# Optimization experiments

Measured on AMD Instinct MI355X. Metric: run time of the kernel, lower is better.

The kernel has to match this reference:

```python
import jax, jax.numpy as jnp
import numpy as np

B, T, C, H, W = 8, 8, 32, 16, 28
NH, DK = 4, 8                 # n_head, d_k == d_v
RADIUS = [3, 3, 3, 3]
DILATION = [1, 3, 5, 7]
LN_EPS = 1e-5


def setup_inputs() -> dict:
    key = jax.random.key(0)
    ks = jax.random.split(key, 8)
    s = 1.0 / np.sqrt(C).astype(np.float32)
    return {
        "first": jax.random.normal(ks[0], (B, T, C, H, W), jnp.float32),
        "x": jax.random.normal(ks[1], (B, T, C, H, W), jnp.float32),
        "Wq": jax.random.normal(ks[2], (NH * DK, C), jnp.float32) * s,
        "Wk": jax.random.normal(ks[3], (NH * DK, C), jnp.float32) * s,
        "Wv": jax.random.normal(ks[4], (NH * DK, C), jnp.float32) * s,
        "Wo": jax.random.normal(ks[5], (C, NH * DK), jnp.float32) * s,
        "ln_gamma": 1.0 + 0.1 * jax.random.normal(ks[6], (DK, H, W), jnp.float32),
        "ln_beta": 0.1 * jax.random.normal(ks[7], (DK, H, W), jnp.float32),
    }


def _shift(x, dy, dx):
    # out[..., i, j] = x[..., i+dy, j+dx]; zero out-of-bounds. mask: (H, W) valid.
    h, w = x.shape[-2:]
    xs = jnp.roll(x, (-dy, -dx), axis=(-2, -1))
    mh = (jnp.arange(h) + dy >= 0) & (jnp.arange(h) + dy < h)
    mw = (jnp.arange(w) + dx >= 0) & (jnp.arange(w) + dx < w)
    m = mh[:, None] & mw[None, :]
    return jnp.where(m, xs, 0.0), m


def _head_attn(q, k, v, radius, dilation, scale):
    # q,k,v: (b,t,c,h,w). Returns softmaxed scores P (b,t,O*t,h,w) and
    # aggregation T (b,t,c,h,w). Aggregation uses RAW scaled scores (as the repo
    # does: spatial_temporal_aggregation receives M_A_i, not its softmax).
    b, t, c, h, w = q.shape
    scores, vals, masks = [], [], []
    for dy in range(-radius, radius + 1):
        for dx in range(-radius, radius + 1):
            ks, m = _shift(k, dy * dilation, dx * dilation)
            vs, _ = _shift(v, dy * dilation, dx * dilation)
            # score against all source frames s at the shifted spatial location
            scores.append(jnp.einsum('btchw,bschw->btshw', q, ks))
            vals.append(vs)
            masks.append(m)
    A = jnp.stack(scores, axis=2)                      # (b,t,O,s,h,w), O=(2r+1)^2
    M = jnp.stack(masks, axis=0)                       # (O,h,w)
    A = jnp.where(M[None, None, :, None], A / scale, -jnp.inf)
    O = A.shape[2]
    P = jax.nn.softmax(A.reshape(b, t, O * t, h, w), axis=2)
    Wm = jnp.where(M[None, None, :, None], A, 0.0)     # skip invalid (-inf) slots
    V = jnp.stack(vals, axis=0)                        # (O,b,s,c,h,w)
    Tout = jnp.einsum('btoshw,obschw->btchw', Wm, V)
    return P, Tout


def reference(first, x, Wq, Wk, Wv, Wo, ln_gamma, ln_beta):
    b, t, c, h, w = x.shape
    q = jnp.einsum('btchw,oc->btohw', first, Wq).reshape(b, t, NH, DK, h, w)
    k = jnp.einsum('btchw,oc->btohw', x, Wk).reshape(b, t, NH, DK, h, w)
    v = jnp.einsum('btchw,oc->btohw', x, Wv).reshape(b, t, NH, DK, h, w)
    scale = float(np.sqrt(C / NH))
    Ps, Ts = [], []
    for i in range(NH):
        qi = q[:, :, i]
        mu = jnp.mean(qi, axis=(2, 3, 4), keepdims=True)
        var = jnp.var(qi, axis=(2, 3, 4), keepdims=True)
        qi = (qi - mu) / jnp.sqrt(var + LN_EPS) * ln_gamma + ln_beta
        P, Ti = _head_attn(qi, k[:, :, i], v[:, :, i], RADIUS[i], DILATION[i], scale)
        Ps.append(P)
        Ts.append(Ti)
    M_S = jnp.max(jnp.concatenate(Ps, axis=2), axis=2)   # (b,t,h,w)
    M_T = jnp.concatenate(Ts, axis=2)                    # (b,t,NH*DK,h,w)
    out = jnp.einsum('btchw,oc->btohw', M_T, Wo) * M_S[:, :, None]
    return out
```

## Files before the change

kernel.cpp:

```cpp
#include <hip/hip_runtime.h>

#define Bc 8
#define Tc 8
#define Cc 32
#define Hc 16
#define Wc 28
#define NHc 4
#define DKc 8
#define HWc (Hc*Wc)
#define INV_SCALE 0.35355339059327373f
#define LN_EPSc 1e-5f

typedef _Float16 half8  __attribute__((ext_vector_type(8)));
typedef _Float16 half2v __attribute__((ext_vector_type(2)));

union H8 { half8 v; half2v h2[4]; };


__global__ __launch_bounds__(448) void qkv_ln_kernel(
    const float* __restrict__ first, const float* __restrict__ x,
    const float* __restrict__ Wq, const float* __restrict__ Wk,
    const float* __restrict__ Wv,
    const float* __restrict__ gamma, const float* __restrict__ beta,
    half8* __restrict__ Qh, half8* __restrict__ Kh, float* __restrict__ V)
{
    int blk  = blockIdx.x;
    int head = blk >> 6;
    int bt   = blk & 63;
    int t    = bt % Tc;
    int b    = bt / Tc;
    int tid  = threadIdx.x;

    const float* fp = first + (size_t)bt * Cc * HWc + tid;
    const float* xp = x     + (size_t)bt * Cc * HWc + tid;
    float fv[Cc], xv[Cc];
#pragma unroll
    for (int c = 0; c < Cc; ++c) { fv[c] = fp[c*HWc]; xv[c] = xp[c*HWc]; }

    float qv[DKc], kv[DKc], vv[DKc];
#pragma unroll
    for (int dk = 0; dk < DKc; ++dk) {
        int o = head*DKc + dk;
        float aq = 0.f, ak = 0.f, av = 0.f;
#pragma unroll
        for (int c = 0; c < Cc; ++c) {
            aq = fmaf(Wq[o*Cc+c], fv[c], aq);
            ak = fmaf(Wk[o*Cc+c], xv[c], ak);
            av = fmaf(Wv[o*Cc+c], xv[c], av);
        }
        qv[dk] = aq; kv[dk] = ak; vv[dk] = av;
    }

    int bh = b*NHc + head;
    half8 kh;
#pragma unroll
    for (int dk = 0; dk < DKc; ++dk) kh[dk] = (_Float16)kv[dk];
    Kh[((size_t)bh*Tc + t)*HWc + tid] = kh;

    float* vp = V + (((size_t)bh*Tc + t)*HWc + tid)*DKc;
    *(float4*)(vp)   = make_float4(vv[0],vv[1],vv[2],vv[3]);
    *(float4*)(vp+4) = make_float4(vv[4],vv[5],vv[6],vv[7]);

    float s1 = 0.f, s2 = 0.f;
#pragma unroll
    for (int dk = 0; dk < DKc; ++dk) { s1 += qv[dk]; s2 += qv[dk]*qv[dk]; }
#pragma unroll
    for (int off = 32; off >= 1; off >>= 1) {
        s1 += __shfl_down(s1, off, 64);
        s2 += __shfl_down(s2, off, 64);
    }
    __shared__ float r1[8], r2[8];
    int wid = tid >> 6, lane = tid & 63;
    if (lane == 0) { r1[wid] = s1; r2[wid] = s2; }
    __syncthreads();
    float S1 = 0.f, S2 = 0.f;
#pragma unroll
    for (int wv2 = 0; wv2 < 7; ++wv2) { S1 += r1[wv2]; S2 += r2[wv2]; }
    const float invN = 1.f / (float)(DKc * HWc);
    float mu   = S1 * invN;
    float var  = S2 * invN - mu*mu;
    float rstd = rsqrtf(var + LN_EPSc);

    half8 qh;
#pragma unroll
    for (int dk = 0; dk < DKc; ++dk) {
        float gg = gamma[dk*HWc + tid];
        float bb = beta [dk*HWc + tid];
        qh[dk] = (_Float16)(((qv[dk] - mu) * rstd * gg + bb) * INV_SCALE);
    }
    Qh[((size_t)bh*Tc + t)*HWc + tid] = qh;
}

__global__ __launch_bounds__(448, 4) void attn_kernel(
    const half8* __restrict__ Qh, const half8* __restrict__ Kh,
    const float* __restrict__ V,
    half8* __restrict__ Tpart, float2* __restrict__ LMpart)
{
    int blk = blockIdx.x;
    int p   = blk >> 8;
    int i   = blk & 255;
    int b   = i >> 5;
    int ha  = (i >> 4) & 1;
    int s   = (i >> 1) & 7;
    int th  = i & 1;

    int head = p ? (3 - ha) : ha;
    int dil  = 2*head + 1;
    int bh   = b*NHc + head;
    int t0   = th*4;

    int tid = threadIdx.x;
    int w = tid % Wc;
    int h = tid / Wc;

    __shared__ half8  sK [HWc+1];
    __shared__ float4 sV0[HWc+1], sV1[HWc+1];

    sK[tid] = Kh[((size_t)bh*Tc + s)*HWc + tid];
    const float* vp = V + ((size_t)bh*Tc + s)*HWc*DKc;
    sV0[tid] = *(const float4*)(vp + tid*DKc);
    sV1[tid] = *(const float4*)(vp + tid*DKc + 4);
    if (tid == 0) {
        half8 z = {};
        sK[HWc]  = z;
        sV0[HWc] = make_float4(0.f,0.f,0.f,0.f);
        sV1[HWc] = make_float4(0.f,0.f,0.f,0.f);
    }

    H8 q[4];
#pragma unroll
    for (int j = 0; j < 4; ++j)
        q[j].v = Qh[((size_t)bh*Tc + (t0+j))*HWc + tid];

    float4 a0[4], a1[4];
    float l[4], m[4];
#pragma unroll
    for (int j = 0; j < 4; ++j) {
        a0[j] = make_float4(0.f,0.f,0.f,0.f);
        a1[j] = make_float4(0.f,0.f,0.f,0.f);
        l[j] = 0.f; m[j] = -1e30f;
    }

    __syncthreads();

    for (int dy = -3; dy <= 3; ++dy) {
        int hy = h + dy*dil;
        if ((unsigned)hy >= (unsigned)Hc) continue;
        int rowbase = hy*Wc;
#pragma unroll
        for (int dx = -3; dx <= 3; ++dx) {
            int wx = w + dx*dil;
            bool cv = (unsigned)wx < (unsigned)Wc;
            int idx = cv ? (rowbase + wx) : HWc;
            float bias = cv ? 0.f : -1e30f;
            H8 k; k.v = sK[idx];
            float4 v0 = sV0[idx], v1 = sV1[idx];
#pragma unroll
            for (int j = 0; j < 4; ++j) {
                float sc = __builtin_amdgcn_fdot2(q[j].h2[0], k.h2[0],
                           __builtin_amdgcn_fdot2(q[j].h2[1], k.h2[1],
                           __builtin_amdgcn_fdot2(q[j].h2[2], k.h2[2],
                           __builtin_amdgcn_fdot2(q[j].h2[3], k.h2[3],
                                                  0.f, false), false), false), false);
                float msc = sc + bias;
                m[j] = fmaxf(m[j], msc);
                l[j] += __expf(msc);
                a0[j].x = fmaf(sc, v0.x, a0[j].x);
                a0[j].y = fmaf(sc, v0.y, a0[j].y);
                a0[j].z = fmaf(sc, v0.z, a0[j].z);
                a0[j].w = fmaf(sc, v0.w, a0[j].w);
                a1[j].x = fmaf(sc, v1.x, a1[j].x);
                a1[j].y = fmaf(sc, v1.y, a1[j].y);
                a1[j].z = fmaf(sc, v1.z, a1[j].z);
                a1[j].w = fmaf(sc, v1.w, a1[j].w);
            }
        }
    }

    half8*  tp  = Tpart  + (size_t)(bh*Tc + s)*Tc*HWc + tid;
    float2* lmp = LMpart + (size_t)(bh*Tc + s)*Tc*HWc + tid;
#pragma unroll
    for (int j = 0; j < 4; ++j) {
        half8 hv;
        hv[0] = (_Float16)a0[j].x; hv[1] = (_Float16)a0[j].y;
        hv[2] = (_Float16)a0[j].z; hv[3] = (_Float16)a0[j].w;
        hv[4] = (_Float16)a1[j].x; hv[5] = (_Float16)a1[j].y;
        hv[6] = (_Float16)a1[j].z; hv[7] = (_Float16)a1[j].w;
        tp [(t0+j)*HWc] = hv;
        lmp[(t0+j)*HWc] = make_float2(l[j], m[j]);
    }
}

__global__ __launch_bounds__(448) void outproj_kernel(
    const half8* __restrict__ Tpart, const float2* __restrict__ LMpart,
    const float* __restrict__ Wo, float* __restrict__ out)
{
    int blk = blockIdx.x;
    int og  = blk >> 6;
    int bt  = blk & 63;
    int b   = bt >> 3, t = bt & 7;
    int tid = threadIdx.x;

    float mv[Cc];
    float MS = 0.f;
#pragma unroll
    for (int head = 0; head < NHc; ++head) {
        int bh = b*NHc + head;
        float acc[DKc];
#pragma unroll
        for (int j = 0; j < DKc; ++j) acc[j] = 0.f;
        float lsum = 0.f, mmax = -1e30f;
#pragma unroll
        for (int s = 0; s < Tc; ++s) {
            half8 u = Tpart[(size_t)((bh*Tc + s)*Tc + t)*HWc + tid];
#pragma unroll
            for (int j = 0; j < DKc; ++j) acc[j] += (float)u[j];
            float2 lm = LMpart[(size_t)((bh*Tc + s)*Tc + t)*HWc + tid];
            lsum += lm.x; mmax = fmaxf(mmax, lm.y);
        }
#pragma unroll
        for (int j = 0; j < DKc; ++j) mv[head*DKc + j] = acc[j];
        MS = fmaxf(MS, __expf(mmax) / lsum);
    }
#pragma unroll
    for (int i = 0; i < 8; ++i) {
        int o = og*8 + i;
        float a = 0.f;
#pragma unroll
        for (int c = 0; c < Cc; ++c) a = fmaf(Wo[o*Cc+c], mv[c], a);
        out[((size_t)bt*Cc + o)*HWc + tid] = a * MS;
    }
}

extern "C" void kernel_launch(void* const* d_in, const int* in_sizes, int n_in,
                              void* d_out, int out_size, void* d_ws, size_t ws_size,
                              hipStream_t stream) {
    const float* first = (const float*)d_in[0];
    const float* x     = (const float*)d_in[1];
    const float* Wq    = (const float*)d_in[2];
    const float* Wk    = (const float*)d_in[3];
    const float* Wv    = (const float*)d_in[4];
    const float* Wo    = (const float*)d_in[5];
    const float* g     = (const float*)d_in[6];
    const float* bta   = (const float*)d_in[7];
    float* out = (float*)d_out;

    float* ws = (float*)d_ws;
    const size_t N5 = (size_t)Bc*NHc*Tc*HWc*DKc;
    half8*  Qh  = (half8*)ws;
    half8*  Kh  = (half8*)(ws + N5/2);
    float*  V   = ws + N5;
    half8*  Tp  = (half8*)(ws + 2*N5);
    float2* LMp = (float2*)(ws + 6*N5);

    qkv_ln_kernel <<<Bc*Tc*NHc, 448, 0, stream>>>(first, x, Wq, Wk, Wv, g, bta, Qh, Kh, V);
    attn_kernel   <<<512,       448, 0, stream>>>(Qh, Kh, V, Tp, LMp);
    outproj_kernel<<<256,       448, 0, stream>>>(Tp, LMp, Wo, out);
}
```

Baseline: 116.0 us.

## Pad shared K/V with zero halo, template dilation, use exp2 and fp16 V

Stores K/V in a zero-padded shared-memory grid so out-of-range horizontal neighbours read zeros, which removes the per-tap bounds check and the -inf bias. The extra exp2(0)=1 terms this adds to the softmax denominator are subtracted analytically using a per-pixel count of invalid taps. The dilation becomes a template parameter so offsets are compile-time constants and the dy loop is fully unrolled. Q is prescaled by log2e so exp2 can be used, with a ln2 factor applied back on the aggregated output, and V is written in fp16 to halve its traffic. The risks are reduced V precision, a larger padded shared-memory footprint that may lower occupancy, and a larger code size from four template instantiations.

```diff
diff --git a/kernel.cpp b/kernel.cpp
--- a/kernel.cpp
+++ b/kernel.cpp
@@ -9,7 +9,18 @@
 #define DKc 8
 #define HWc (Hc*Wc)
 #define INV_SCALE 0.35355339059327373f
+#define LOG2E 1.4426950408889634f
+#define LN2f 0.6931471805599453f
 #define LN_EPSc 1e-5f
+
+#define WPAD 70
+#define NSLOT (Hc*WPAD)
+
+#if __has_builtin(__builtin_amdgcn_exp2f)
+#define EXP2f(x) __builtin_amdgcn_exp2f(x)
+#else
+#define EXP2f(x) exp2f(x)
+#endif
 
 typedef _Float16 half8  __attribute__((ext_vector_type(8)));
 typedef _Float16 half2v __attribute__((ext_vector_type(2)));
@@ -22,7 +33,7 @@
     const float* __restrict__ Wq, const float* __restrict__ Wk,
     const float* __restrict__ Wv,
     const float* __restrict__ gamma, const float* __restrict__ beta,
-    half8* __restrict__ Qh, half8* __restrict__ Kh, float* __restrict__ V)
+    half8* __restrict__ Qh, half8* __restrict__ Kh, half8* __restrict__ Vh)
 {
     int blk  = blockIdx.x;
     int head = blk >> 6;
@@ -52,14 +63,14 @@
     }
 
     int bh = b*NHc + head;
-    half8 kh;
-#pragma unroll
-    for (int dk = 0; dk < DKc; ++dk) kh[dk] = (_Float16)kv[dk];
+    half8 kh, vh;
+#pragma unroll
+    for (int dk = 0; dk < DKc; ++dk) {
+        kh[dk] = (_Float16)kv[dk];
+        vh[dk] = (_Float16)vv[dk];
+    }
     Kh[((size_t)bh*Tc + t)*HWc + tid] = kh;
-
-    float* vp = V + (((size_t)bh*Tc + t)*HWc + tid)*DKc;
-    *(float4*)(vp)   = make_float4(vv[0],vv[1],vv[2],vv[3]);
-    *(float4*)(vp+4) = make_float4(vv[4],vv[5],vv[6],vv[7]);
+    Vh[((size_t)bh*Tc + t)*HWc + tid] = vh;
 
     float s1 = 0.f, s2 = 0.f;
 #pragma unroll
@@ -81,80 +92,76 @@
     float var  = S2 * invN - mu*mu;
     float rstd = rsqrtf(var + LN_EPSc);
 
+    const float QSCALE = INV_SCALE * LOG2E;
     half8 qh;
 #pragma unroll
     for (int dk = 0; dk < DKc; ++dk) {
         float gg = gamma[dk*HWc + tid];
         float bb = beta [dk*HWc + tid];
-        qh[dk] = (_Float16)(((qv[dk] - mu) * rstd * gg + bb) * INV_SCALE);
+        qh[dk] = (_Float16)(((qv[dk] - mu) * rstd * gg + bb) * QSCALE);
     }
     Qh[((size_t)bh*Tc + t)*HWc + tid] = qh;
 }
 
-__global__ __launch_bounds__(448, 4) void attn_kernel(
+template<int DIL>
+__device__ __forceinline__ void attn_body(
+    int bh, int s, int t0, int tid,
     const half8* __restrict__ Qh, const half8* __restrict__ Kh,
-    const float* __restrict__ V,
-    half8* __restrict__ Tpart, float2* __restrict__ LMpart)
-{
-    int blk = blockIdx.x;
-    int p   = blk >> 8;
-    int i   = blk & 255;
-    int b   = i >> 5;
-    int ha  = (i >> 4) & 1;
-    int s   = (i >> 1) & 7;
-    int th  = i & 1;
-
-    int head = p ? (3 - ha) : ha;
-    int dil  = 2*head + 1;
-    int bh   = b*NHc + head;
-    int t0   = th*4;
-
-    int tid = threadIdx.x;
+    const half8* __restrict__ Vh,
+    half8* __restrict__ Tpart, float2* __restrict__ LMpart,
+    half8* sK, float4* sV0, float4* sV1)
+{
     int w = tid % Wc;
     int h = tid / Wc;
 
-    __shared__ half8  sK [HWc+1];
-    __shared__ float4 sV0[HWc+1], sV1[HWc+1];
-
-    sK[tid] = Kh[((size_t)bh*Tc + s)*HWc + tid];
-    const float* vp = V + ((size_t)bh*Tc + s)*HWc*DKc;
-    sV0[tid] = *(const float4*)(vp + tid*DKc);
-    sV1[tid] = *(const float4*)(vp + tid*DKc + 4);
-    if (tid == 0) {
-        half8 z = {};
-        sK[HWc]  = z;
-        sV0[HWc] = make_float4(0.f,0.f,0.f,0.f);
-        sV1[HWc] = make_float4(0.f,0.f,0.f,0.f);
-    }
+    half8 z = {};
+    float4 zf = make_float4(0.f,0.f,0.f,0.f);
+    for (int p = tid; p < NSLOT; p += 448) { sK[p] = z; sV0[p] = zf; sV1[p] = zf; }
+    __syncthreads();
+
+    int slot = h*WPAD + 21 + w;
+    sK[slot] = Kh[((size_t)bh*Tc + s)*HWc + tid];
+    H8 v8; v8.v = Vh[((size_t)bh*Tc + s)*HWc + tid];
+    sV0[slot] = make_float4((float)v8.v[0], (float)v8.v[1],
+                            (float)v8.v[2], (float)v8.v[3]);
+    sV1[slot] = make_float4((float)v8.v[4], (float)v8.v[5],
+                            (float)v8.v[6], (float)v8.v[7]);
 
     H8 q[4];
 #pragma unroll
     for (int j = 0; j < 4; ++j)
         q[j].v = Qh[((size_t)bh*Tc + (t0+j))*HWc + tid];
 
+    int nvy = 0, nvx = 0;
+#pragma unroll
+    for (int d = -3; d <= 3; ++d) {
+        nvy += ((unsigned)(h + d*DIL) < (unsigned)Hc);
+        nvx += ((unsigned)(w + d*DIL) < (unsigned)Wc);
+    }
+    float corr = (float)(nvy * (7 - nvx));
+
     float4 a0[4], a1[4];
     float l[4], m[4];
 #pragma unroll
     for (int j = 0; j < 4; ++j) {
-        a0[j] = make_float4(0.f,0.f,0.f,0.f);
-        a1[j] = make_float4(0.f,0.f,0.f,0.f);
+        a0[j] = zf; a1[j] = zf;
         l[j] = 0.f; m[j] = -1e30f;
     }
 
     __syncthreads();
 
+#pragma unroll
     for (int dy = -3; dy <= 3; ++dy) {
-        int hy = h + dy*dil;
+        int hy = h + dy*DIL;
         if ((unsigned)hy >= (unsigned)Hc) continue;
-        int rowbase = hy*Wc;
-#pragma unroll
-        for (int dx = -3; dx <= 3; ++dx) {
-            int wx = w + dx*dil;
-            bool cv = (unsigned)wx < (unsigned)Wc;
-            int idx = cv ? (rowbase + wx) : HWc;
-            float bias = cv ? 0.f : -1e30f;
-            H8 k; k.v = sK[idx];
-            float4 v0 = sV0[idx], v1 = sV1[idx];
+        int rb = hy*WPAD + (w + 21 - 3*DIL);
+        const half8*  kp  = sK  + rb;
+        const float4* v0p = sV0 + rb;
+        const float4* v1p = sV1 + rb;
+#pragma unroll
+        for (int dx = 0; dx < 7; ++dx) {
+            H8 k; k.v = kp[dx*DIL];
+            float4 v0 = v0p[dx*DIL], v1 = v1p[dx*DIL];
 #pragma unroll
             for (int j = 0; j < 4; ++j) {
                 float sc = __builtin_amdgcn_fdot2(q[j].h2[0], k.h2[0],
@@ -162,9 +169,8 @@
                            __builtin_amdgcn_fdot2(q[j].h2[2], k.h2[2],
                            __builtin_amdgcn_fdot2(q[j].h2[3], k.h2[3],
                                                   0.f, false), false), false), false);
-                float msc = sc + bias;
-                m[j] = fmaxf(m[j], msc);
-                l[j] += __expf(msc);
+                m[j] = fmaxf(m[j], sc);
+                l[j] += EXP2f(sc);
                 a0[j].x = fmaf(sc, v0.x, a0[j].x);
                 a0[j].y = fmaf(sc, v0.y, a0[j].y);
                 a0[j].z = fmaf(sc, v0.z, a0[j].z);
@@ -182,13 +188,40 @@
 #pragma unroll
     for (int j = 0; j < 4; ++j) {
         half8 hv;
-        hv[0] = (_Float16)a0[j].x; hv[1] = (_Float16)a0[j].y;
-        hv[2] = (_Float16)a0[j].z; hv[3] = (_Float16)a0[j].w;
-        hv[4] = (_Float16)a1[j].x; hv[5] = (_Float16)a1[j].y;
-        hv[6] = (_Float16)a1[j].z; hv[7] = (_Float16)a1[j].w;
+        hv[0] = (_Float16)(a0[j].x * LN2f); hv[1] = (_Float16)(a0[j].y * LN2f);
+        hv[2] = (_Float16)(a0[j].z * LN2f); hv[3] = (_Float16)(a0[j].w * LN2f);
+        hv[4] = (_Float16)(a1[j].x * LN2f); hv[5] = (_Float16)(a1[j].y * LN2f);
+        hv[6] = (_Float16)(a1[j].z * LN2f); hv[7] = (_Float16)(a1[j].w * LN2f);
         tp [(t0+j)*HWc] = hv;
-        lmp[(t0+j)*HWc] = make_float2(l[j], m[j]);
-    }
+        lmp[(t0+j)*HWc] = make_float2(l[j] - corr, m[j]);
+    }
+}
+
+__global__ __launch_bounds__(448, 4) void attn_kernel(
+    const half8* __restrict__ Qh, const half8* __restrict__ Kh,
+    const half8* __restrict__ Vh,
+    half8* __restrict__ Tpart, float2* __restrict__ LMpart)
+{
+    int blk = blockIdx.x;
+    int p   = blk >> 8;
+    int i   = blk & 255;
+    int b   = i >> 5;
+    int ha  = (i >> 4) & 1;
+    int s   = (i >> 1) & 7;
+    int th  = i & 1;
+
+    int head = p ? (3 - ha) : ha;
+    int bh   = b*NHc + head;
+    int t0   = th*4;
+    int tid  = threadIdx.x;
+
+    __shared__ half8  sK [NSLOT];
+    __shared__ float4 sV0[NSLOT], sV1[NSLOT];
+
+    if      (head == 0) attn_body<1>(bh, s, t0, tid, Qh, Kh, Vh, Tpart, LMpart, sK, sV0, sV1);
+    else if (head == 1) attn_body<3>(bh, s, t0, tid, Qh, Kh, Vh, Tpart, LMpart, sK, sV0, sV1);
+    else if (head == 2) attn_body<5>(bh, s, t0, tid, Qh, Kh, Vh, Tpart, LMpart, sK, sV0, sV1);
+    else                attn_body<7>(bh, s, t0, tid, Qh, Kh, Vh, Tpart, LMpart, sK, sV0, sV1);
 }
 
 __global__ __launch_bounds__(448) void outproj_kernel(
@@ -220,7 +253,7 @@
         }
 #pragma unroll
         for (int j = 0; j < DKc; ++j) mv[head*DKc + j] = acc[j];
-        MS = fmaxf(MS, __expf(mmax) / lsum);
+        MS = fmaxf(MS, EXP2f(mmax) / lsum);
     }
 #pragma unroll
     for (int i = 0; i < 8; ++i) {
@@ -249,11 +282,11 @@
     const size_t N5 = (size_t)Bc*NHc*Tc*HWc*DKc;
     half8*  Qh  = (half8*)ws;
     half8*  Kh  = (half8*)(ws + N5/2);
-    float*  V   = ws + N5;
-    half8*  Tp  = (half8*)(ws + 2*N5);
-    float2* LMp = (float2*)(ws + 6*N5);
-
-    qkv_ln_kernel <<<Bc*Tc*NHc, 448, 0, stream>>>(first, x, Wq, Wk, Wv, g, bta, Qh, Kh, V);
-    attn_kernel   <<<512,       448, 0, stream>>>(Qh, Kh, V, Tp, LMp);
+    half8*  Vh  = (half8*)(ws + N5);
+    half8*  Tp  = (half8*)(ws + 3*N5/2);
+    float2* LMp = (float2*)(ws + 3*N5/2 + 4*N5);
+
+    qkv_ln_kernel <<<Bc*Tc*NHc, 448, 0, stream>>>(first, x, Wq, Wk, Wv, g, bta, Qh, Kh, Vh);
+    attn_kernel   <<<512,       448, 0, stream>>>(Qh, Kh, Vh, Tp, LMp);
     outproj_kernel<<<256,       448, 0, stream>>>(Tp, LMp, Wo, out);
 }
```

Measured after the change: 121.2 us. 4.5% more time.

## Specialize attention on dilation, use exp2 with log2e-folded scores, packed FMAs

Applied to the files above, without the earlier changes.

Folds log2(e) into the Q scaling so the softmax sum can use the native exp2 instruction, and rescales the aggregation by ln2 at the end. Masked out-of-bounds columns no longer get a -1e30 bias. Their exp(0)=1 contributions are subtracted analytically through a per-pixel count of invalid offsets. The attention body is templated on dilation so the loops fully unroll with constant offsets, and the V accumulation uses packed float2 FMAs. Together these aim to cut per-offset ALU work in the hot loop. The cost is more code and register pressure, plus a small precision risk from scaling before the fp16 cast.

```diff
diff --git a/kernel.cpp b/kernel.cpp
--- a/kernel.cpp
+++ b/kernel.cpp
@@ -9,12 +9,22 @@
 #define DKc 8
 #define HWc (Hc*Wc)
 #define INV_SCALE 0.35355339059327373f
+#define LOG2E 1.4426950408889634f
+#define LN2f 0.6931471805599453f
 #define LN_EPSc 1e-5f
+
+#if __has_builtin(__builtin_amdgcn_exp2f)
+#define EXP2f(x) __builtin_amdgcn_exp2f(x)
+#else
+#define EXP2f(x) exp2f(x)
+#endif
 
 typedef _Float16 half8  __attribute__((ext_vector_type(8)));
 typedef _Float16 half2v __attribute__((ext_vector_type(2)));
+typedef float    f2     __attribute__((ext_vector_type(2)));
 
 union H8 { half8 v; half2v h2[4]; };
+union F4 { float4 f4; f2 p[2]; };
 
 
 __global__ __launch_bounds__(448) void qkv_ln_kernel(
@@ -81,40 +91,27 @@
     float var  = S2 * invN - mu*mu;
     float rstd = rsqrtf(var + LN_EPSc);
 
+    const float QSCALE = INV_SCALE * LOG2E;
     half8 qh;
 #pragma unroll
     for (int dk = 0; dk < DKc; ++dk) {
         float gg = gamma[dk*HWc + tid];
         float bb = beta [dk*HWc + tid];
-        qh[dk] = (_Float16)(((qv[dk] - mu) * rstd * gg + bb) * INV_SCALE);
+        qh[dk] = (_Float16)(((qv[dk] - mu) * rstd * gg + bb) * QSCALE);
     }
     Qh[((size_t)bh*Tc + t)*HWc + tid] = qh;
 }
 
-__global__ __launch_bounds__(448, 4) void attn_kernel(
+template<int DIL>
+__device__ __forceinline__ void attn_body(
+    int bh, int s, int t0, int tid,
     const half8* __restrict__ Qh, const half8* __restrict__ Kh,
     const float* __restrict__ V,
-    half8* __restrict__ Tpart, float2* __restrict__ LMpart)
-{
-    int blk = blockIdx.x;
-    int p   = blk >> 8;
-    int i   = blk & 255;
-    int b   = i >> 5;
-    int ha  = (i >> 4) & 1;
-    int s   = (i >> 1) & 7;
-    int th  = i & 1;
-
-    int head = p ? (3 - ha) : ha;
-    int dil  = 2*head + 1;
-    int bh   = b*NHc + head;
-    int t0   = th*4;
-
-    int tid = threadIdx.x;
+    half8* __restrict__ Tpart, float2* __restrict__ LMpart,
+    half8* sK, float4* sV0, float4* sV1)
+{
     int w = tid % Wc;
     int h = tid / Wc;
-
-    __shared__ half8  sK [HWc+1];
-    __shared__ float4 sV0[HWc+1], sV1[HWc+1];
 
     sK[tid] = Kh[((size_t)bh*Tc + s)*HWc + tid];
     const float* vp = V + ((size_t)bh*Tc + s)*HWc*DKc;
@@ -132,29 +129,37 @@
     for (int j = 0; j < 4; ++j)
         q[j].v = Qh[((size_t)bh*Tc + (t0+j))*HWc + tid];
 
-    float4 a0[4], a1[4];
+    int nvy = 0, nvx = 0;
+#pragma unroll
+    for (int d = -3; d <= 3; ++d) {
+        nvy += ((unsigned)(h + d*DIL) < (unsigned)Hc);
+        nvx += ((unsigned)(w + d*DIL) < (unsigned)Wc);
+    }
+    float corr = (float)(nvy * (7 - nvx));
+
+    f2 a[4][4];
     float l[4], m[4];
 #pragma unroll
     for (int j = 0; j < 4; ++j) {
-        a0[j] = make_float4(0.f,0.f,0.f,0.f);
-        a1[j] = make_float4(0.f,0.f,0.f,0.f);
+#pragma unroll
+        for (int u = 0; u < 4; ++u) a[j][u] = (f2){0.f, 0.f};
         l[j] = 0.f; m[j] = -1e30f;
     }
 
     __syncthreads();
 
+#pragma unroll
     for (int dy = -3; dy <= 3; ++dy) {
-        int hy = h + dy*dil;
+        int hy = h + dy*DIL;
         if ((unsigned)hy >= (unsigned)Hc) continue;
         int rowbase = hy*Wc;
 #pragma unroll
         for (int dx = -3; dx <= 3; ++dx) {
-            int wx = w + dx*dil;
+            int wx = w + dx*DIL;
             bool cv = (unsigned)wx < (unsigned)Wc;
             int idx = cv ? (rowbase + wx) : HWc;
-            float bias = cv ? 0.f : -1e30f;
             H8 k; k.v = sK[idx];
-            float4 v0 = sV0[idx], v1 = sV1[idx];
+            F4 v0, v1; v0.f4 = sV0[idx]; v1.f4 = sV1[idx];
 #pragma unroll
             for (int j = 0; j < 4; ++j) {
                 float sc = __builtin_amdgcn_fdot2(q[j].h2[0], k.h2[0],
@@ -162,17 +167,13 @@
                            __builtin_amdgcn_fdot2(q[j].h2[2], k.h2[2],
                            __builtin_amdgcn_fdot2(q[j].h2[3], k.h2[3],
                                                   0.f, false), false), false), false);
-                float msc = sc + bias;
-                m[j] = fmaxf(m[j], msc);
-                l[j] += __expf(msc);
-                a0[j].x = fmaf(sc, v0.x, a0[j].x);
-                a0[j].y = fmaf(sc, v0.y, a0[j].y);
-                a0[j].z = fmaf(sc, v0.z, a0[j].z);
-                a0[j].w = fmaf(sc, v0.w, a0[j].w);
-                a1[j].x = fmaf(sc, v1.x, a1[j].x);
-                a1[j].y = fmaf(sc, v1.y, a1[j].y);
-                a1[j].z = fmaf(sc, v1.z, a1[j].z);
-                a1[j].w = fmaf(sc, v1.w, a1[j].w);
+                m[j] = fmaxf(m[j], sc);
+                l[j] += EXP2f(sc);
+                f2 sc2 = {sc, sc};
+                a[j][0] = __builtin_elementwise_fma(sc2, v0.p[0], a[j][0]);
+                a[j][1] = __builtin_elementwise_fma(sc2, v0.p[1], a[j][1]);
+                a[j][2] = __builtin_elementwise_fma(sc2, v1.p[0], a[j][2]);
+                a[j][3] = __builtin_elementwise_fma(sc2, v1.p[1], a[j][3]);
             }
         }
     }
@@ -182,13 +183,41 @@
 #pragma unroll
     for (int j = 0; j < 4; ++j) {
         half8 hv;
-        hv[0] = (_Float16)a0[j].x; hv[1] = (_Float16)a0[j].y;
-        hv[2] = (_Float16)a0[j].z; hv[3] = (_Float16)a0[j].w;
-        hv[4] = (_Float16)a1[j].x; hv[5] = (_Float16)a1[j].y;
-        hv[6] = (_Float16)a1[j].z; hv[7] = (_Float16)a1[j].w;
+#pragma unroll
+        for (int u = 0; u < 4; ++u) {
+            hv[2*u]   = (_Float16)(a[j][u][0] * LN2f);
+            hv[2*u+1] = (_Float16)(a[j][u][1] * LN2f);
+        }
         tp [(t0+j)*HWc] = hv;
-        lmp[(t0+j)*HWc] = make_float2(l[j], m[j]);
-    }
+        lmp[(t0+j)*HWc] = make_float2(l[j] - corr, m[j]);
+    }
+}
+
+__global__ __launch_bounds__(448, 4) void attn_kernel(
+    const half8* __restrict__ Qh, const half8* __restrict__ Kh,
+    const float* __restrict__ V,
+    half8* __restrict__ Tpart, float2* __restrict__ LMpart)
+{
+    int blk = blockIdx.x;
+    int p   = blk >> 8;
+    int i   = blk & 255;
+    int b   = i >> 5;
+    int ha  = (i >> 4) & 1;
+    int s   = (i >> 1) & 7;
+    int th  = i & 1;
+
+    int head = p ? (3 - ha) : ha;
+    int bh   = b*NHc + head;
+    int t0   = th*4;
+    int tid  = threadIdx.x;
+
+    __shared__ half8  sK [HWc+1];
+    __shared__ float4 sV0[HWc+1], sV1[HWc+1];
+
+    if      (head == 0) attn_body<1>(bh, s, t0, tid, Qh, Kh, V, Tpart, LMpart, sK, sV0, sV1);
+    else if (head == 1) attn_body<3>(bh, s, t0, tid, Qh, Kh, V, Tpart, LMpart, sK, sV0, sV1);
+    else if (head == 2) attn_body<5>(bh, s, t0, tid, Qh, Kh, V, Tpart, LMpart, sK, sV0, sV1);
+    else                attn_body<7>(bh, s, t0, tid, Qh, Kh, V, Tpart, LMpart, sK, sV0, sV1);
 }
 
 __global__ __launch_bounds__(448) void outproj_kernel(
@@ -220,7 +249,7 @@
         }
 #pragma unroll
         for (int j = 0; j < DKc; ++j) mv[head*DKc + j] = acc[j];
-        MS = fmaxf(MS, __expf(mmax) / lsum);
+        MS = fmaxf(MS, EXP2f(mmax) / lsum);
     }
 #pragma unroll
     for (int i = 0; i < 8; ++i) {
```

Result: faster. 113.0 us (-2.6%).
